# Kernel tuning notes

Measured on AMD Instinct MI355X. Metric: run time of the kernel, lower is better.

Reference implementation:

```python
import jax, jax.numpy as jnp
import numpy as np

N_NODES = 50000
N_EDGES = 800000
N_GRAPHS = 500
IN_DIM = 128
HID = 96
OUT_DIM = 64


def _lin(k, fan_in, fan_out):
    return jax.random.normal(k, (fan_in, fan_out), jnp.float32) / np.float32(np.sqrt(fan_in))


def setup_inputs() -> dict:
    key = jax.random.key(0)
    ks = jax.random.split(key, 12)
    x = jax.random.normal(ks[0], (N_NODES, IN_DIM), jnp.float32)
    edge_index = jax.random.randint(ks[1], (2, N_EDGES), 0, N_NODES)
    batch = jnp.sort(jax.random.randint(ks[2], (N_NODES,), 0, N_GRAPHS))
    return {
        "x": x,
        "edge_index": edge_index,
        "batch": batch,
        # GCN conv weights (first: in->hid, rest: hid->hid)
        "W0": _lin(ks[3], IN_DIM, HID), "b0": jnp.zeros((HID,), jnp.float32),
        "W1": _lin(ks[4], HID, HID),    "b1": jnp.zeros((HID,), jnp.float32),
        "W2": _lin(ks[5], HID, HID),    "b2": jnp.zeros((HID,), jnp.float32),
        # jumping-knowledge 'cat' projection: 3*hid -> hid
        "Wjk": _lin(ks[6], 3 * HID, HID), "bjk": jnp.zeros((HID,), jnp.float32),
        # fc_o MLP: hid -> hid -> out
        "Wm1": _lin(ks[7], HID, HID),   "bm1": jnp.zeros((HID,), jnp.float32),
        "Wm2": _lin(ks[8], HID, OUT_DIM), "bm2": jnp.zeros((OUT_DIM,), jnp.float32),
    }


def reference(x, edge_index, batch, W0, b0, W1, b1, W2, b2, Wjk, bjk, Wm1, bm1, Wm2, bm2):
    n = x.shape[0]
    loop = jnp.arange(n, dtype=edge_index.dtype)
    src = jnp.concatenate([edge_index[0], loop])  # [E+N] with self-loops
    dst = jnp.concatenate([edge_index[1], loop])
    # symmetric GCN normalization: D^{-1/2} (A+I) D^{-1/2}
    deg = jax.ops.segment_sum(jnp.ones_like(dst, x.dtype), dst, num_segments=n)
    dinv = jax.lax.rsqrt(jnp.maximum(deg, 1.0))  # deg >= 1 with self-loops
    norm = dinv[src] * dinv[dst]  # [E+N]

    def gcn_conv(h, W, b):
        m = (h @ W)[src] * norm[:, None]                      # gather + scale
        return jax.ops.segment_sum(m, dst, num_segments=n) + b  # scatter-add

    h1 = jax.nn.relu(gcn_conv(x, W0, b0))
    h2 = jax.nn.relu(gcn_conv(h1, W1, b1))
    h3 = jax.nn.relu(gcn_conv(h2, W2, b2))
    # JK 'cat' + final linear (PyG BasicGNN lin)
    h = jnp.concatenate([h1, h2, h3], axis=-1) @ Wjk + bjk    # [N, HID]
    # global add pooling over graphs
    emb_o = jax.ops.segment_sum(h, batch, num_segments=N_GRAPHS)  # [G, HID]
    # fc_o MLP (eval: dropout/identity-batchnorm omitted)
    pred_o = jax.nn.relu(emb_o @ Wm1 + bm1) @ Wm2 + bm2       # [G, OUT]
    return pred_o
```

## Files before the change

### kernel.cpp

```cpp
#include <hip/hip_runtime.h>
#include <hip/hip_fp16.h>

#define NN 50000
#define NE 800000
#define NG 500
#define IND 128
#define HD 96
#define OD 64

#define SCAN_CHUNK 2048
#define SCAN_BLOCKS ((NN + SCAN_CHUNK - 1) / SCAN_CHUNK)


__global__ void zero_k(int* __restrict__ cnt) {
  int i = blockIdx.x * 256 + threadIdx.x;
  if (i < NN) cnt[i] = 0;
}

__global__ void hist_k(const int* __restrict__ dst, int* __restrict__ cnt,
                       int* __restrict__ rank) {
  int i0 = (blockIdx.x * 256 + threadIdx.x) * 8;
  if (i0 + 8 <= NE) {
    int4 d0 = *reinterpret_cast<const int4*>(&dst[i0]);
    int4 d1 = *reinterpret_cast<const int4*>(&dst[i0 + 4]);
    int4 r0, r1;
    r0.x = atomicAdd(&cnt[d0.x], 1);
    r0.y = atomicAdd(&cnt[d0.y], 1);
    r0.z = atomicAdd(&cnt[d0.z], 1);
    r0.w = atomicAdd(&cnt[d0.w], 1);
    r1.x = atomicAdd(&cnt[d1.x], 1);
    r1.y = atomicAdd(&cnt[d1.y], 1);
    r1.z = atomicAdd(&cnt[d1.z], 1);
    r1.w = atomicAdd(&cnt[d1.w], 1);
    *reinterpret_cast<int4*>(&rank[i0]) = r0;
    *reinterpret_cast<int4*>(&rank[i0 + 4]) = r1;
  } else {
    for (int i = i0; i < NE; i++) rank[i] = atomicAdd(&cnt[dst[i]], 1);
  }
}

__global__ __launch_bounds__(256) void scan_part_k(const int* __restrict__ cnt,
                                                   int* __restrict__ bsum,
                                                   float* __restrict__ dinv) {
  __shared__ int ts[256];
  const int tid = threadIdx.x;
  const int base = blockIdx.x * SCAN_CHUNK + tid * 8;
  int s = 0;
#pragma unroll
  for (int j = 0; j < 8; j++) {
    int idx = base + j;
    if (idx < NN) {
      int c = cnt[idx];
      s += c;
      dinv[idx] = rsqrtf((float)(c + 1));
    }
  }
  ts[tid] = s;
  __syncthreads();
  for (int off = 128; off > 0; off >>= 1) {
    if (tid < off) ts[tid] += ts[tid + off];
    __syncthreads();
  }
  if (tid == 0) bsum[blockIdx.x] = ts[0];
}

__global__ __launch_bounds__(64) void scan_top_k(const int* __restrict__ bsum,
                                                 int* __restrict__ boff,
                                                 int* __restrict__ row_ptr) {
  int tid = threadIdx.x;
  int v = (tid < SCAN_BLOCKS) ? bsum[tid] : 0;
  for (int off = 1; off < 64; off <<= 1) {
    int u = __shfl_up(v, off);
    if (tid >= off) v += u;
  }
  if (tid < SCAN_BLOCKS) boff[tid] = v - bsum[tid];
  if (tid == 0) row_ptr[NN] = NE;
}

__global__ __launch_bounds__(256) void scan_fin_k(const int* __restrict__ cnt,
                                                  const int* __restrict__ boff,
                                                  int* __restrict__ row_ptr) {
  __shared__ int ts[256];
  const int tid = threadIdx.x;
  const int base = blockIdx.x * SCAN_CHUNK + tid * 8;
  int v[8];
  int s = 0;
#pragma unroll
  for (int j = 0; j < 8; j++) {
    int idx = base + j;
    v[j] = (idx < NN) ? cnt[idx] : 0;
    s += v[j];
  }
  ts[tid] = s;
  __syncthreads();
  for (int off = 1; off < 256; off <<= 1) {
    int t = (tid >= off) ? ts[tid - off] : 0;
    __syncthreads();
    ts[tid] += t;
    __syncthreads();
  }
  int run = ((tid == 0) ? 0 : ts[tid - 1]) + boff[blockIdx.x];
#pragma unroll
  for (int j = 0; j < 8; j++) {
    int idx = base + j;
    if (idx < NN) row_ptr[idx] = run;
    run += v[j];
  }
}

__global__ void fill_k(const int* __restrict__ src, const int* __restrict__ dst,
                       const int* __restrict__ row_ptr, const int* __restrict__ rank,
                       int* __restrict__ col) {
  int i0 = (blockIdx.x * 256 + threadIdx.x) * 8;
  if (i0 + 8 <= NE) {
    int4 d0 = *reinterpret_cast<const int4*>(&dst[i0]);
    int4 d1 = *reinterpret_cast<const int4*>(&dst[i0 + 4]);
    int4 s0 = *reinterpret_cast<const int4*>(&src[i0]);
    int4 s1 = *reinterpret_cast<const int4*>(&src[i0 + 4]);
    int4 r0 = *reinterpret_cast<const int4*>(&rank[i0]);
    int4 r1 = *reinterpret_cast<const int4*>(&rank[i0 + 4]);
    int p0 = row_ptr[d0.x], p1 = row_ptr[d0.y], p2 = row_ptr[d0.z], p3 = row_ptr[d0.w];
    int p4 = row_ptr[d1.x], p5 = row_ptr[d1.y], p6 = row_ptr[d1.z], p7 = row_ptr[d1.w];
    col[p0 + r0.x] = s0.x * (HD * 2);
    col[p1 + r0.y] = s0.y * (HD * 2);
    col[p2 + r0.z] = s0.z * (HD * 2);
    col[p3 + r0.w] = s0.w * (HD * 2);
    col[p4 + r1.x] = s1.x * (HD * 2);
    col[p5 + r1.y] = s1.y * (HD * 2);
    col[p6 + r1.z] = s1.z * (HD * 2);
    col[p7 + r1.w] = s1.w * (HD * 2);
  } else {
    for (int i = i0; i < NE; i++)
      col[row_ptr[dst[i]] + rank[i]] = src[i] * (HD * 2);
  }
}

template <int K, typename T>
__global__ __launch_bounds__(256) void gemm_scale_k(const T* __restrict__ h,
                                                    const float* __restrict__ W,
                                                    const float* __restrict__ dinv,
                                                    __half* __restrict__ g) {
  __shared__ float hsT[32][66];
  __shared__ __attribute__((aligned(16))) float ws[32][100];
  const int tid = threadIdx.x;
  const int rowg = tid >> 3;
  const int colg = tid & 7;
  const int row0 = blockIdx.x * 64;

  float acc[2][12];
#pragma unroll
  for (int i = 0; i < 2; i++)
#pragma unroll
    for (int j = 0; j < 12; j++) acc[i][j] = 0.f;

  for (int k0 = 0; k0 < K; k0 += 32) {
    if constexpr (sizeof(T) == 4) {
#pragma unroll
      for (int lin = tid; lin < 512; lin += 256) {
        int r = lin >> 3, q = lin & 7;
        int grow = row0 + r;
        float4 v = make_float4(0.f, 0.f, 0.f, 0.f);
        if (grow < NN)
          v = *reinterpret_cast<const float4*>(&h[(long)grow * K + k0 + 4 * q]);
        hsT[4 * q + 0][r] = v.x;
        hsT[4 * q + 1][r] = v.y;
        hsT[4 * q + 2][r] = v.z;
        hsT[4 * q + 3][r] = v.w;
      }
    } else {
      int r = tid >> 2, q = tid & 3;
      int grow = row0 + r;
      if (grow < NN) {
        int4 raw = *reinterpret_cast<const int4*>(
            reinterpret_cast<const __half*>(h) + (long)grow * K + k0 + 8 * q);
        const __half2* hp = reinterpret_cast<const __half2*>(&raw);
#pragma unroll
        for (int t = 0; t < 4; t++) {
          float2 f = __half22float2(hp[t]);
          hsT[8 * q + 2 * t + 0][r] = f.x;
          hsT[8 * q + 2 * t + 1][r] = f.y;
        }
      } else {
#pragma unroll
        for (int t = 0; t < 8; t++) hsT[8 * q + t][r] = 0.f;
      }
    }
#pragma unroll
    for (int lin = tid; lin < 768; lin += 256) {
      int kk = lin / 24, c4 = lin - kk * 24;
      *reinterpret_cast<float4*>(&ws[kk][4 * c4]) =
          *reinterpret_cast<const float4*>(&W[(long)(k0 + kk) * HD + 4 * c4]);
    }
    __syncthreads();
#pragma unroll 8
    for (int k = 0; k < 32; k++) {
      float2 a = *reinterpret_cast<const float2*>(&hsT[k][2 * rowg]);
      float4 w0 = *reinterpret_cast<const float4*>(&ws[k][12 * colg]);
      float4 w1 = *reinterpret_cast<const float4*>(&ws[k][12 * colg + 4]);
      float4 w2 = *reinterpret_cast<const float4*>(&ws[k][12 * colg + 8]);
      float wv[12] = {w0.x, w0.y, w0.z, w0.w, w1.x, w1.y, w1.z, w1.w,
                      w2.x, w2.y, w2.z, w2.w};
      float av[2] = {a.x, a.y};
#pragma unroll
      for (int i = 0; i < 2; i++)
#pragma unroll
        for (int j = 0; j < 12; j++) acc[i][j] = fmaf(av[i], wv[j], acc[i][j]);
    }
    __syncthreads();
  }
#pragma unroll
  for (int i = 0; i < 2; i++) {
    int row = row0 + 2 * rowg + i;
    if (row < NN) {
      float dv = dinv[row];
      __half2 hh[6];
#pragma unroll
      for (int q = 0; q < 6; q++)
        hh[q] = __floats2half2_rn(acc[i][2 * q] * dv, acc[i][2 * q + 1] * dv);
      __half* go = g + (long)row * HD + 12 * colg;
      *reinterpret_cast<float2*>(go) = *reinterpret_cast<float2*>(&hh[0]);
      *reinterpret_cast<float2*>(go + 4) = *reinterpret_cast<float2*>(&hh[2]);
      *reinterpret_cast<float2*>(go + 8) = *reinterpret_cast<float2*>(&hh[4]);
    }
  }
}

__global__ __launch_bounds__(256) void gather_k(const __half* __restrict__ g,
                                                const int* __restrict__ row_ptr,
                                                const int* __restrict__ col,
                                                const float* __restrict__ dinv,
                                                const float* __restrict__ bias,
                                                __half* __restrict__ hout) {
  int d = blockIdx.x * 4 + (threadIdx.x >> 6);
  int lane = threadIdx.x & 63;
  if (d >= NN) return;
  const bool active = (lane < 48);
  const int s = active ? (lane / 12) : 0;
  const int c = active ? (lane % 12) : 0;
  const int cofs = 16 * c;
  const char* gb = reinterpret_cast<const char*>(g);
  const int own = d * (HD * 2);

  float acc[8];
#pragma unroll
  for (int k = 0; k < 8; k++) acc[k] = 0.f;

  {
    float4 raw = *reinterpret_cast<const float4*>(gb + own + cofs);
    const __half2* hp = reinterpret_cast<const __half2*>(&raw);
    float m = (active && s == 0) ? 1.f : 0.f;
#pragma unroll
    for (int q = 0; q < 4; q++) {
      float2 f = __half22float2(hp[q]);
      acc[2 * q + 0] = fmaf(m, f.x, acc[2 * q + 0]);
      acc[2 * q + 1] = fmaf(m, f.y, acc[2 * q + 1]);
    }
  }

  int e = row_ptr[d];
  const int end = row_ptr[d + 1];
  while (e < end) {
    int cnt = end - e; if (cnt > 64) cnt = 64;
    int cid = (lane < cnt) ? col[e + lane] : own;
    int j = 0;
    for (; j + 16 <= cnt; j += 16) {
      int o0 = __shfl(cid, j + s);
      int o1 = __shfl(cid, j + 4 + s);
      int o2 = __shfl(cid, j + 8 + s);
      int o3 = __shfl(cid, j + 12 + s);
      float4 r0 = *reinterpret_cast<const float4*>(gb + o0 + cofs);
      float4 r1 = *reinterpret_cast<const float4*>(gb + o1 + cofs);
      float4 r2 = *reinterpret_cast<const float4*>(gb + o2 + cofs);
      float4 r3 = *reinterpret_cast<const float4*>(gb + o3 + cofs);
      const __half2* h0 = reinterpret_cast<const __half2*>(&r0);
      const __half2* h1 = reinterpret_cast<const __half2*>(&r1);
      const __half2* h2 = reinterpret_cast<const __half2*>(&r2);
      const __half2* h3 = reinterpret_cast<const __half2*>(&r3);
#pragma unroll
      for (int q = 0; q < 4; q++) {
        float2 f0 = __half22float2(h0[q]);
        float2 f1 = __half22float2(h1[q]);
        float2 f2 = __half22float2(h2[q]);
        float2 f3 = __half22float2(h3[q]);
        acc[2 * q + 0] += (f0.x + f1.x) + (f2.x + f3.x);
        acc[2 * q + 1] += (f0.y + f1.y) + (f2.y + f3.y);
      }
    }
    for (; j < cnt; j += 4) {
      int o = __shfl(cid, j + s);
      float m = (j + s < cnt) ? 1.f : 0.f;
      float4 r = *reinterpret_cast<const float4*>(gb + o + cofs);
      const __half2* hp = reinterpret_cast<const __half2*>(&r);
#pragma unroll
      for (int q = 0; q < 4; q++) {
        float2 f = __half22float2(hp[q]);
        acc[2 * q + 0] = fmaf(m, f.x, acc[2 * q + 0]);
        acc[2 * q + 1] = fmaf(m, f.y, acc[2 * q + 1]);
      }
    }
    e += 64;
  }

#pragma unroll
  for (int k = 0; k < 8; k++) acc[k] += __shfl(acc[k], lane + 24);
#pragma unroll
  for (int k = 0; k < 8; k++) acc[k] += __shfl(acc[k], lane + 12);

  if (lane < 12) {
    float dv = dinv[d];
    float4 b0 = *reinterpret_cast<const float4*>(&bias[8 * c]);
    float4 b1 = *reinterpret_cast<const float4*>(&bias[8 * c + 4]);
    float vb[8] = {b0.x, b0.y, b0.z, b0.w, b1.x, b1.y, b1.z, b1.w};
    __half2 hh[4];
#pragma unroll
    for (int q = 0; q < 4; q++) {
      float v0 = fmaxf(fmaf(acc[2 * q + 0], dv, vb[2 * q + 0]), 0.f);
      float v1 = fmaxf(fmaf(acc[2 * q + 1], dv, vb[2 * q + 1]), 0.f);
      hh[q] = __floats2half2_rn(v0, v1);
    }
    *reinterpret_cast<float4*>(&hout[(long)d * HD + 8 * c]) =
        *reinterpret_cast<float4*>(hh);
  }
}

__global__ __launch_bounds__(256) void head_k(const __half* __restrict__ hA,
                                              const __half* __restrict__ hB,
                                              const __half* __restrict__ hC,
                                              const int* __restrict__ batch,
                                              const float* __restrict__ Wjk,
                                              const float* __restrict__ bjk,
                                              const float* __restrict__ Wm1,
                                              const float* __restrict__ bm1,
                                              const float* __restrict__ Wm2,
                                              const float* __restrict__ bm2,
                                              float* __restrict__ out) {
  __shared__ float red[240][12];
  __shared__ float p1[HD], p2[HD], p3[HD], se[HD], shid[HD];
  const int g = blockIdx.x;
  const int t = threadIdx.x;

  int lo = 0, hi = NN;
  while (lo < hi) { int mid = (lo + hi) >> 1; if (batch[mid] < g) lo = mid + 1; else hi = mid; }
  const int n0 = lo;
  lo = 0; hi = NN;
  while (lo < hi) { int mid = (lo + hi) >> 1; if (batch[mid] < g + 1) lo = mid + 1; else hi = mid; }
  const int n1 = lo;

  const int q = t % 24, s = t / 24;
  if (t < 240) {
    float aA[4] = {0.f, 0.f, 0.f, 0.f}, aB[4] = {0.f, 0.f, 0.f, 0.f},
          aC[4] = {0.f, 0.f, 0.f, 0.f};
    for (int n = n0 + s; n < n1; n += 10) {
      float2 rA = *reinterpret_cast<const float2*>(&hA[(long)n * HD + 4 * q]);
      float2 rB = *reinterpret_cast<const float2*>(&hB[(long)n * HD + 4 * q]);
      float2 rC = *reinterpret_cast<const float2*>(&hC[(long)n * HD + 4 * q]);
      const __half2* pA = reinterpret_cast<const __half2*>(&rA);
      const __half2* pB = reinterpret_cast<const __half2*>(&rB);
      const __half2* pC = reinterpret_cast<const __half2*>(&rC);
#pragma unroll
      for (int u = 0; u < 2; u++) {
        float2 fA = __half22float2(pA[u]);
        float2 fB = __half22float2(pB[u]);
        float2 fC = __half22float2(pC[u]);
        aA[2 * u] += fA.x; aA[2 * u + 1] += fA.y;
        aB[2 * u] += fB.x; aB[2 * u + 1] += fB.y;
        aC[2 * u] += fC.x; aC[2 * u + 1] += fC.y;
      }
    }
#pragma unroll
    for (int u = 0; u < 4; u++) {
      red[t][u] = aA[u];
      red[t][4 + u] = aB[u];
      red[t][8 + u] = aC[u];
    }
  }
  __syncthreads();
  if (t < 24) {
    float sum[12];
#pragma unroll
    for (int u = 0; u < 12; u++) sum[u] = 0.f;
    for (int ss = 0; ss < 10; ss++)
#pragma unroll
      for (int u = 0; u < 12; u++) sum[u] += red[ss * 24 + t][u];
#pragma unroll
    for (int k = 0; k < 4; k++) {
      p1[4 * t + k] = sum[k];
      p2[4 * t + k] = sum[4 + k];
      p3[4 * t + k] = sum[8 + k];
    }
  }
  __syncthreads();

  if (t < HD) {
    float acc = (float)(n1 - n0) * bjk[t];
    for (int k = 0; k < HD; k++) {
      acc = fmaf(p1[k], Wjk[k * HD + t], acc);
      acc = fmaf(p2[k], Wjk[(HD + k) * HD + t], acc);
      acc = fmaf(p3[k], Wjk[(2 * HD + k) * HD + t], acc);
    }
    se[t] = acc;
  }
  __syncthreads();
  if (t < HD) {
    float acc = bm1[t];
    for (int k = 0; k < HD; k++) acc = fmaf(se[k], Wm1[k * HD + t], acc);
    shid[t] = fmaxf(acc, 0.f);
  }
  __syncthreads();
  if (t < OD) {
    float acc = bm2[t];
    for (int k = 0; k < HD; k++) acc = fmaf(shid[k], Wm2[k * OD + t], acc);
    out[g * OD + t] = acc;
  }
}


extern "C" void kernel_launch(void* const* d_in, const int* in_sizes, int n_in,
                              void* d_out, int out_size, void* d_ws, size_t ws_size,
                              hipStream_t stream) {
  const float* x = (const float*)d_in[0];
  const int* ei = (const int*)d_in[1];
  const int* batch = (const int*)d_in[2];
  const float* W0 = (const float*)d_in[3];  const float* b0 = (const float*)d_in[4];
  const float* W1 = (const float*)d_in[5];  const float* b1 = (const float*)d_in[6];
  const float* W2 = (const float*)d_in[7];  const float* b2 = (const float*)d_in[8];
  const float* Wjk = (const float*)d_in[9]; const float* bjk = (const float*)d_in[10];
  const float* Wm1 = (const float*)d_in[11]; const float* bm1 = (const float*)d_in[12];
  const float* Wm2 = (const float*)d_in[13]; const float* bm2 = (const float*)d_in[14];
  const int* srcp = ei;
  const int* dstp = ei + NE;

  char* wp = (char*)d_ws;
  size_t off = 0;
  auto alloc = [&](size_t bytes) -> void* {
    void* p = wp + off;
    off += bytes;
    off = (off + 255) & ~(size_t)255;
    return p;
  };
  int* cnt    = (int*)alloc((size_t)NN * 4);
  int* rowp   = (int*)alloc((size_t)(NN + 1) * 4);
  int* rank   = (int*)alloc((size_t)NE * 4);
  int* colb   = (int*)alloc((size_t)NE * 4);
  float* dinv = (float*)alloc((size_t)NN * 4);
  int* bsum   = (int*)alloc((size_t)SCAN_BLOCKS * 4);
  int* boff   = (int*)alloc((size_t)SCAN_BLOCKS * 4);
  __half* g   = (__half*)alloc((size_t)NN * HD * 2);
  __half* hA  = (__half*)alloc((size_t)NN * HD * 2);
  __half* hB  = (__half*)alloc((size_t)NN * HD * 2);
  __half* hC  = (__half*)alloc((size_t)NN * HD * 2);

  zero_k<<<(NN + 255) / 256, 256, 0, stream>>>(cnt);

  const int eb8 = (NE / 8 + 255) / 256;
  hist_k<<<eb8, 256, 0, stream>>>(dstp, cnt, rank);
  scan_part_k<<<SCAN_BLOCKS, 256, 0, stream>>>(cnt, bsum, dinv);
  scan_top_k<<<1, 64, 0, stream>>>(bsum, boff, rowp);
  scan_fin_k<<<SCAN_BLOCKS, 256, 0, stream>>>(cnt, boff, rowp);
  fill_k<<<eb8, 256, 0, stream>>>(srcp, dstp, rowp, rank, colb);

  const int gemm_grid = (NN + 63) / 64;
  const int gath_grid = (NN + 3) / 4;
  gemm_scale_k<IND, float><<<gemm_grid, 256, 0, stream>>>(x, W0, dinv, g);
  gather_k<<<gath_grid, 256, 0, stream>>>(g, rowp, colb, dinv, b0, hA);
  gemm_scale_k<HD, __half><<<gemm_grid, 256, 0, stream>>>(hA, W1, dinv, g);
  gather_k<<<gath_grid, 256, 0, stream>>>(g, rowp, colb, dinv, b1, hB);
  gemm_scale_k<HD, __half><<<gemm_grid, 256, 0, stream>>>(hB, W2, dinv, g);
  gather_k<<<gath_grid, 256, 0, stream>>>(g, rowp, colb, dinv, b2, hC);

  head_k<<<NG, 256, 0, stream>>>(hA, hB, hC, batch, Wjk, bjk, Wm1, bm1, Wm2, bm2,
                                 (float*)d_out);
}
```

Measured before the change: 240.1 us.

## Use MFMA fp16 for node GEMMs and 16-bit CSR rank/col indices

Rewrites the per-layer dense GEMM to use MFMA 16x16x32 fp16 instructions, with the whole weight matrix packed into LDS as fp16, replacing the fp32 FMA tiled loop. It also narrows the edge rank and column-index arrays from 32-bit to 16-bit to cut memory traffic in the histogram, fill and gather kernels. Node ids go up to 50000, which fits in unsigned short, but this only holds for this node count. Converting inputs and weights to fp16 lowers GEMM precision, and the epilogue now writes single halves instead of vector stores.

Result: faster. 213.6 us (-11.0%).

```diff
diff --git a/kernel.cpp b/kernel.cpp
--- a/kernel.cpp
+++ b/kernel.cpp
@@ -11,6 +11,9 @@
 #define SCAN_CHUNK 2048
 #define SCAN_BLOCKS ((NN + SCAN_CHUNK - 1) / SCAN_CHUNK)
 
+typedef _Float16 f16x8 __attribute__((ext_vector_type(8)));
+typedef float f32x4 __attribute__((ext_vector_type(4)));
+
 
 __global__ void zero_k(int* __restrict__ cnt) {
   int i = blockIdx.x * 256 + threadIdx.x;
@@ -18,24 +21,24 @@
 }
 
 __global__ void hist_k(const int* __restrict__ dst, int* __restrict__ cnt,
-                       int* __restrict__ rank) {
+                       unsigned short* __restrict__ rank) {
   int i0 = (blockIdx.x * 256 + threadIdx.x) * 8;
   if (i0 + 8 <= NE) {
     int4 d0 = *reinterpret_cast<const int4*>(&dst[i0]);
     int4 d1 = *reinterpret_cast<const int4*>(&dst[i0 + 4]);
-    int4 r0, r1;
-    r0.x = atomicAdd(&cnt[d0.x], 1);
-    r0.y = atomicAdd(&cnt[d0.y], 1);
-    r0.z = atomicAdd(&cnt[d0.z], 1);
-    r0.w = atomicAdd(&cnt[d0.w], 1);
-    r1.x = atomicAdd(&cnt[d1.x], 1);
-    r1.y = atomicAdd(&cnt[d1.y], 1);
-    r1.z = atomicAdd(&cnt[d1.z], 1);
-    r1.w = atomicAdd(&cnt[d1.w], 1);
-    *reinterpret_cast<int4*>(&rank[i0]) = r0;
-    *reinterpret_cast<int4*>(&rank[i0 + 4]) = r1;
+    alignas(16) unsigned short r[8];
+    r[0] = (unsigned short)atomicAdd(&cnt[d0.x], 1);
+    r[1] = (unsigned short)atomicAdd(&cnt[d0.y], 1);
+    r[2] = (unsigned short)atomicAdd(&cnt[d0.z], 1);
+    r[3] = (unsigned short)atomicAdd(&cnt[d0.w], 1);
+    r[4] = (unsigned short)atomicAdd(&cnt[d1.x], 1);
+    r[5] = (unsigned short)atomicAdd(&cnt[d1.y], 1);
+    r[6] = (unsigned short)atomicAdd(&cnt[d1.z], 1);
+    r[7] = (unsigned short)atomicAdd(&cnt[d1.w], 1);
+    *reinterpret_cast<int4*>(&rank[i0]) = *reinterpret_cast<int4*>(r);
   } else {
-    for (int i = i0; i < NE; i++) rank[i] = atomicAdd(&cnt[dst[i]], 1);
+    for (int i = i0; i < NE; i++)
+      rank[i] = (unsigned short)atomicAdd(&cnt[dst[i]], 1);
   }
 }
 
@@ -109,29 +112,30 @@
 }
 
 __global__ void fill_k(const int* __restrict__ src, const int* __restrict__ dst,
-                       const int* __restrict__ row_ptr, const int* __restrict__ rank,
-                       int* __restrict__ col) {
+                       const int* __restrict__ row_ptr,
+                       const unsigned short* __restrict__ rank,
+                       unsigned short* __restrict__ col) {
   int i0 = (blockIdx.x * 256 + threadIdx.x) * 8;
   if (i0 + 8 <= NE) {
     int4 d0 = *reinterpret_cast<const int4*>(&dst[i0]);
     int4 d1 = *reinterpret_cast<const int4*>(&dst[i0 + 4]);
     int4 s0 = *reinterpret_cast<const int4*>(&src[i0]);
     int4 s1 = *reinterpret_cast<const int4*>(&src[i0 + 4]);
-    int4 r0 = *reinterpret_cast<const int4*>(&rank[i0]);
-    int4 r1 = *reinterpret_cast<const int4*>(&rank[i0 + 4]);
+    alignas(16) unsigned short r[8];
+    *reinterpret_cast<int4*>(r) = *reinterpret_cast<const int4*>(&rank[i0]);
     int p0 = row_ptr[d0.x], p1 = row_ptr[d0.y], p2 = row_ptr[d0.z], p3 = row_ptr[d0.w];
     int p4 = row_ptr[d1.x], p5 = row_ptr[d1.y], p6 = row_ptr[d1.z], p7 = row_ptr[d1.w];
-    col[p0 + r0.x] = s0.x * (HD * 2);
-    col[p1 + r0.y] = s0.y * (HD * 2);
-    col[p2 + r0.z] = s0.z * (HD * 2);
-    col[p3 + r0.w] = s0.w * (HD * 2);
-    col[p4 + r1.x] = s1.x * (HD * 2);
-    col[p5 + r1.y] = s1.y * (HD * 2);
-    col[p6 + r1.z] = s1.z * (HD * 2);
-    col[p7 + r1.w] = s1.w * (HD * 2);
+    col[p0 + r[0]] = (unsigned short)s0.x;
+    col[p1 + r[1]] = (unsigned short)s0.y;
+    col[p2 + r[2]] = (unsigned short)s0.z;
+    col[p3 + r[3]] = (unsigned short)s0.w;
+    col[p4 + r[4]] = (unsigned short)s1.x;
+    col[p5 + r[5]] = (unsigned short)s1.y;
+    col[p6 + r[6]] = (unsigned short)s1.z;
+    col[p7 + r[7]] = (unsigned short)s1.w;
   } else {
     for (int i = i0; i < NE; i++)
-      col[row_ptr[dst[i]] + rank[i]] = src[i] * (HD * 2);
+      col[row_ptr[dst[i]] + rank[i]] = (unsigned short)src[i];
   }
 }
 
@@ -140,94 +144,76 @@
                                                     const float* __restrict__ W,
                                                     const float* __restrict__ dinv,
                                                     __half* __restrict__ g) {
-  __shared__ float hsT[32][66];
-  __shared__ __attribute__((aligned(16))) float ws[32][100];
+  __shared__ __attribute__((aligned(16))) _Float16 wpack[K * HD];
   const int tid = threadIdx.x;
-  const int rowg = tid >> 3;
-  const int colg = tid & 7;
-  const int row0 = blockIdx.x * 64;
-
-  float acc[2][12];
-#pragma unroll
-  for (int i = 0; i < 2; i++)
-#pragma unroll
-    for (int j = 0; j < 12; j++) acc[i][j] = 0.f;
-
-  for (int k0 = 0; k0 < K; k0 += 32) {
-    if constexpr (sizeof(T) == 4) {
-#pragma unroll
-      for (int lin = tid; lin < 512; lin += 256) {
-        int r = lin >> 3, q = lin & 7;
-        int grow = row0 + r;
-        float4 v = make_float4(0.f, 0.f, 0.f, 0.f);
-        if (grow < NN)
-          v = *reinterpret_cast<const float4*>(&h[(long)grow * K + k0 + 4 * q]);
-        hsT[4 * q + 0][r] = v.x;
-        hsT[4 * q + 1][r] = v.y;
-        hsT[4 * q + 2][r] = v.z;
-        hsT[4 * q + 3][r] = v.w;
+  for (int lin = tid; lin < K * (HD / 4); lin += 256) {
+    int k = lin / (HD / 4), n4 = lin - k * (HD / 4);
+    float4 v = *reinterpret_cast<const float4*>(&W[(long)k * HD + 4 * n4]);
+    int base = (k >> 3) * (HD * 8) + (k & 7);
+    wpack[base + (4 * n4 + 0) * 8] = (_Float16)v.x;
+    wpack[base + (4 * n4 + 1) * 8] = (_Float16)v.y;
+    wpack[base + (4 * n4 + 2) * 8] = (_Float16)v.z;
+    wpack[base + (4 * n4 + 3) * 8] = (_Float16)v.w;
+  }
+  __syncthreads();
+
+  const int lane = tid & 63;
+  const int wid = tid >> 6;
+  const int r16 = lane & 15;
+  const int kg = lane >> 4;
+  const int row_base = blockIdx.x * 64 + wid * 16;
+  const int arow = row_base + r16;
+
+  f32x4 acc[6];
+#pragma unroll
+  for (int t = 0; t < 6; t++) acc[t] = (f32x4){0.f, 0.f, 0.f, 0.f};
+
+#pragma unroll
+  for (int kc = 0; kc < K / 32; kc++) {
+    f16x8 a;
+    if (arow < NN) {
+      if constexpr (sizeof(T) == 4) {
+        const float* ap = h + (long)arow * K + kc * 32 + kg * 8;
+        float4 v0 = *reinterpret_cast<const float4*>(ap);
+        float4 v1 = *reinterpret_cast<const float4*>(ap + 4);
+        a[0] = (_Float16)v0.x; a[1] = (_Float16)v0.y;
+        a[2] = (_Float16)v0.z; a[3] = (_Float16)v0.w;
+        a[4] = (_Float16)v1.x; a[5] = (_Float16)v1.y;
+        a[6] = (_Float16)v1.z; a[7] = (_Float16)v1.w;
+      } else {
+        a = *reinterpret_cast<const f16x8*>(
+            reinterpret_cast<const __half*>(h) + (long)arow * K + kc * 32 + kg * 8);
       }
     } else {
-      int r = tid >> 2, q = tid & 3;
-      int grow = row0 + r;
-      if (grow < NN) {
-        int4 raw = *reinterpret_cast<const int4*>(
-            reinterpret_cast<const __half*>(h) + (long)grow * K + k0 + 8 * q);
-        const __half2* hp = reinterpret_cast<const __half2*>(&raw);
-#pragma unroll
-        for (int t = 0; t < 4; t++) {
-          float2 f = __half22float2(hp[t]);
-          hsT[8 * q + 2 * t + 0][r] = f.x;
-          hsT[8 * q + 2 * t + 1][r] = f.y;
-        }
-      } else {
-#pragma unroll
-        for (int t = 0; t < 8; t++) hsT[8 * q + t][r] = 0.f;
-      }
-    }
-#pragma unroll
-    for (int lin = tid; lin < 768; lin += 256) {
-      int kk = lin / 24, c4 = lin - kk * 24;
-      *reinterpret_cast<float4*>(&ws[kk][4 * c4]) =
-          *reinterpret_cast<const float4*>(&W[(long)(k0 + kk) * HD + 4 * c4]);
-    }
-    __syncthreads();
-#pragma unroll 8
-    for (int k = 0; k < 32; k++) {
-      float2 a = *reinterpret_cast<const float2*>(&hsT[k][2 * rowg]);
-      float4 w0 = *reinterpret_cast<const float4*>(&ws[k][12 * colg]);
-      float4 w1 = *reinterpret_cast<const float4*>(&ws[k][12 * colg + 4]);
-      float4 w2 = *reinterpret_cast<const float4*>(&ws[k][12 * colg + 8]);
-      float wv[12] = {w0.x, w0.y, w0.z, w0.w, w1.x, w1.y, w1.z, w1.w,
-                      w2.x, w2.y, w2.z, w2.w};
-      float av[2] = {a.x, a.y};
-#pragma unroll
-      for (int i = 0; i < 2; i++)
-#pragma unroll
-        for (int j = 0; j < 12; j++) acc[i][j] = fmaf(av[i], wv[j], acc[i][j]);
-    }
-    __syncthreads();
-  }
-#pragma unroll
-  for (int i = 0; i < 2; i++) {
-    int row = row0 + 2 * rowg + i;
+#pragma unroll
+      for (int e = 0; e < 8; e++) a[e] = (_Float16)0.f;
+    }
+#pragma unroll
+    for (int t = 0; t < 6; t++) {
+      f16x8 b = *reinterpret_cast<const f16x8*>(
+          &wpack[(kc * 4 + kg) * (HD * 8) + (t * 16 + r16) * 8]);
+      acc[t] = __builtin_amdgcn_mfma_f32_16x16x32_f16(a, b, acc[t], 0, 0, 0);
+    }
+  }
+
+  float dv[4];
+  int rb = row_base + kg * 4;
+#pragma unroll
+  for (int e = 0; e < 4; e++) dv[e] = (rb + e < NN) ? dinv[rb + e] : 0.f;
+#pragma unroll
+  for (int e = 0; e < 4; e++) {
+    int row = rb + e;
     if (row < NN) {
-      float dv = dinv[row];
-      __half2 hh[6];
-#pragma unroll
-      for (int q = 0; q < 6; q++)
-        hh[q] = __floats2half2_rn(acc[i][2 * q] * dv, acc[i][2 * q + 1] * dv);
-      __half* go = g + (long)row * HD + 12 * colg;
-      *reinterpret_cast<float2*>(go) = *reinterpret_cast<float2*>(&hh[0]);
-      *reinterpret_cast<float2*>(go + 4) = *reinterpret_cast<float2*>(&hh[2]);
-      *reinterpret_cast<float2*>(go + 8) = *reinterpret_cast<float2*>(&hh[4]);
+      __half* go = g + (long)row * HD + r16;
+#pragma unroll
+      for (int t = 0; t < 6; t++) go[t * 16] = __float2half(acc[t][e] * dv[e]);
     }
   }
 }
 
 __global__ __launch_bounds__(256) void gather_k(const __half* __restrict__ g,
                                                 const int* __restrict__ row_ptr,
-                                                const int* __restrict__ col,
+                                                const unsigned short* __restrict__ col,
                                                 const float* __restrict__ dinv,
                                                 const float* __restrict__ bias,
                                                 __half* __restrict__ hout) {
@@ -239,14 +225,13 @@
   const int c = active ? (lane % 12) : 0;
   const int cofs = 16 * c;
   const char* gb = reinterpret_cast<const char*>(g);
-  const int own = d * (HD * 2);
 
   float acc[8];
 #pragma unroll
   for (int k = 0; k < 8; k++) acc[k] = 0.f;
 
   {
-    float4 raw = *reinterpret_cast<const float4*>(gb + own + cofs);
+    float4 raw = *reinterpret_cast<const float4*>(gb + d * (HD * 2) + cofs);
     const __half2* hp = reinterpret_cast<const __half2*>(&raw);
     float m = (active && s == 0) ? 1.f : 0.f;
 #pragma unroll
@@ -261,13 +246,13 @@
   const int end = row_ptr[d + 1];
   while (e < end) {
     int cnt = end - e; if (cnt > 64) cnt = 64;
-    int cid = (lane < cnt) ? col[e + lane] : own;
+    int cid = (lane < cnt) ? (int)col[e + lane] : d;
     int j = 0;
     for (; j + 16 <= cnt; j += 16) {
-      int o0 = __shfl(cid, j + s);
-      int o1 = __shfl(cid, j + 4 + s);
-      int o2 = __shfl(cid, j + 8 + s);
-      int o3 = __shfl(cid, j + 12 + s);
+      int o0 = __shfl(cid, j + s) * (HD * 2);
+      int o1 = __shfl(cid, j + 4 + s) * (HD * 2);
+      int o2 = __shfl(cid, j + 8 + s) * (HD * 2);
+      int o3 = __shfl(cid, j + 12 + s) * (HD * 2);
       float4 r0 = *reinterpret_cast<const float4*>(gb + o0 + cofs);
       float4 r1 = *reinterpret_cast<const float4*>(gb + o1 + cofs);
       float4 r2 = *reinterpret_cast<const float4*>(gb + o2 + cofs);
@@ -287,7 +272,7 @@
       }
     }
     for (; j < cnt; j += 4) {
-      int o = __shfl(cid, j + s);
+      int o = __shfl(cid, j + s) * (HD * 2);
       float m = (j + s < cnt) ? 1.f : 0.f;
       float4 r = *reinterpret_cast<const float4*>(gb + o + cofs);
       const __half2* hp = reinterpret_cast<const __half2*>(&r);
@@ -440,8 +425,8 @@
   };
   int* cnt    = (int*)alloc((size_t)NN * 4);
   int* rowp   = (int*)alloc((size_t)(NN + 1) * 4);
-  int* rank   = (int*)alloc((size_t)NE * 4);
-  int* colb   = (int*)alloc((size_t)NE * 4);
+  unsigned short* rank = (unsigned short*)alloc((size_t)NE * 2);
+  unsigned short* colb = (unsigned short*)alloc((size_t)NE * 2);
   float* dinv = (float*)alloc((size_t)NN * 4);
   int* bsum   = (int*)alloc((size_t)SCAN_BLOCKS * 4);
   int* boff   = (int*)alloc((size_t)SCAN_BLOCKS * 4);
```
